# Optimization experiments

Hardware: AMD Instinct MI355X
Metric: run time of the kernel (lower is better)

## Reference

```python
import jax, jax.numpy as jnp
import numpy as np

B, N, F_IN, H, MH, STEPS = 8192, 9, 15, 128, 256, 4
E_PER = 16
MASK_IDX = jnp.arange(8)  # mask = [True]*8 + [False]


def setup_inputs() -> dict:
    key = jax.random.key(0)
    ks = jax.random.split(key, 24)
    s = 0.05
    inp = {
        "obs": jax.random.normal(ks[0], (B, 135), jnp.float32),
        "edges": jax.random.randint(ks[1], (B, 2, E_PER), 0, N, jnp.int32),
        "enc_W": jax.random.normal(ks[2], (F_IN, H), jnp.float32) * s,
        "enc_b": jax.random.normal(ks[3], (H,), jnp.float32) * s,
        "msg_W1": jax.random.normal(ks[4], (STEPS, 2 * H, MH), jnp.float32) * s,
        "msg_b1": jax.random.normal(ks[5], (STEPS, MH), jnp.float32) * s,
        "msg_W2": jax.random.normal(ks[6], (STEPS, MH, MH), jnp.float32) * s,
        "msg_b2": jax.random.normal(ks[7], (STEPS, MH), jnp.float32) * s,
        "msg_W3": jax.random.normal(ks[8], (STEPS, MH, H), jnp.float32) * s,
        "msg_b3": jax.random.normal(ks[9], (STEPS, H), jnp.float32) * s,
        "gru_Wi": jax.random.normal(ks[10], (STEPS, H, 3 * H), jnp.float32) * s,
        "gru_Wh": jax.random.normal(ks[11], (STEPS, H, 3 * H), jnp.float32) * s,
        "gru_bi": jax.random.normal(ks[12], (STEPS, 3 * H), jnp.float32) * s,
        "gru_bh": jax.random.normal(ks[13], (STEPS, 3 * H), jnp.float32) * s,
        "dec_W1": jax.random.normal(ks[14], (H, MH), jnp.float32) * s,
        "dec_b1": jax.random.normal(ks[15], (MH,), jnp.float32) * s,
        "dec_W2": jax.random.normal(ks[16], (MH, MH), jnp.float32) * s,
        "dec_b2": jax.random.normal(ks[17], (MH,), jnp.float32) * s,
        "dec_W3": jax.random.normal(ks[18], (MH, 1), jnp.float32) * s,
        "dec_b3": jax.random.normal(ks[19], (1,), jnp.float32) * s,
    }
    return inp


def reference(obs, edges, enc_W, enc_b, msg_W1, msg_b1, msg_W2, msg_b2,
              msg_W3, msg_b3, gru_Wi, gru_Wh, gru_bi, gru_bh,
              dec_W1, dec_b1, dec_W2, dec_b2, dec_W3, dec_b3):
    BN = B * N
    x = obs.reshape(BN, F_IN)                       # [B*N, 15]
    x = jnp.tanh(x @ enc_W + enc_b)                 # encoder -> [B*N, H]

    # flatten per-graph edges into a global edge list, then add self-loops
    offsets = (jnp.arange(B, dtype=jnp.int32) * N)[:, None, None]
    eg = edges + offsets                            # [B, 2, 16]
    loops = jnp.arange(BN, dtype=jnp.int32)
    src = jnp.concatenate([eg[:, 0, :].reshape(-1), loops])  # x_j (source)
    dst = jnp.concatenate([eg[:, 1, :].reshape(-1), loops])  # x_i (target)
    deg = jax.ops.segment_sum(jnp.ones_like(dst, dtype=x.dtype), dst,
                              num_segments=BN)      # >=1 due to self-loops

    for s in range(STEPS):
        m = jnp.concatenate([x[dst], x[src]], axis=-1)       # [E, 2H]
        m = jnp.tanh(m @ msg_W1[s] + msg_b1[s])
        m = jnp.tanh(m @ msg_W2[s] + msg_b2[s])
        m = m @ msg_W3[s] + msg_b3[s]                        # [E, H]
        aggr = jax.ops.segment_sum(m, dst, num_segments=BN) / deg[:, None]
        # GRUCell(input=aggr, hidden=x), PyTorch gate order (r, z, n)
        gi = aggr @ gru_Wi[s] + gru_bi[s]
        gh = x @ gru_Wh[s] + gru_bh[s]
        ir, iz, inn = jnp.split(gi, 3, axis=-1)
        hr, hz, hn = jnp.split(gh, 3, axis=-1)
        r = jax.nn.sigmoid(ir + hr)
        z = jax.nn.sigmoid(iz + hz)
        n = jnp.tanh(inn + r * hn)
        x = (1.0 - z) * n + z * x

    d = jnp.tanh(x @ dec_W1 + dec_b1)
    d = jnp.tanh(d @ dec_W2 + dec_b2)
    d = d @ dec_W3 + dec_b3                                  # [B*N, 1]
    out = d.reshape(B, N)
    return out[:, MASK_IDX]                                  # [B, 8]
```

## Files before the change

kernel.cpp:

```cpp
#include <hip/hip_runtime.h>
#include <hip/hip_bf16.h>
#include <math.h>

#define BGR   8192
#define NND   9
#define BN    73728
#define NE    131072
#define ETOT  204800
#define H     128
#define MH    256
#define FIN   15

typedef __bf16 bf16_t;
typedef bf16_t bf16x8 __attribute__((ext_vector_type(8)));
typedef float  f32x4  __attribute__((ext_vector_type(4)));
typedef float  f32x16 __attribute__((ext_vector_type(16)));

__device__ __forceinline__ unsigned short f2bf(float f) {
    unsigned int u = __float_as_uint(f);
    u += 0x7fff + ((u >> 16) & 1);
    return (unsigned short)(u >> 16);
}
__device__ __forceinline__ unsigned int pkbf(float a, float b) {
    union { __hip_bfloat162 h; unsigned int u; } un;
    un.h = __float22bfloat162_rn(make_float2(a, b));
    return un.u;
}
__device__ __forceinline__ bf16x8 as_frag(int4 v) {
    union { int4 i; bf16x8 f; } u; u.i = v; return u.f;
}
__device__ __forceinline__ float fast_tanh(float v) {
    float e = __expf(2.0f * v);
    return 1.0f - __fdividef(2.0f, e + 1.0f);
}
__device__ __forceinline__ int sw16(int m, int k) {
    return m * 256 + ((((k >> 3) ^ (m & 15)) << 3) | (k & 7));
}
__device__ __forceinline__ int swp(int m, int k) {
    return m * 128 + ((((k >> 3) ^ (m & 15)) << 3) | (k & 7));
}
__device__ __forceinline__ int sw_off(int m, int k) {
    return m * 256 + ((((k >> 3) ^ (m & 7)) << 3) | (k & 7));
}

__global__ void deg_kernel(const int* __restrict__ edges, float* __restrict__ inv_deg) {
    int g = blockIdx.x * 256 + threadIdx.x;
    if (g >= BGR) return;
    int cnt[NND];
#pragma unroll
    for (int n = 0; n < NND; ++n) cnt[n] = 1;
    for (int j = 0; j < 16; ++j) {
        int d = edges[g * 32 + 16 + j];
#pragma unroll
        for (int n = 0; n < NND; ++n) cnt[n] += (d == n) ? 1 : 0;
    }
#pragma unroll
    for (int n = 0; n < NND; ++n) inv_deg[g * NND + n] = 1.0f / (float)cnt[n];
}

__global__ void enc_kernel(const float* __restrict__ obs, const float* __restrict__ W,
                           const float* __restrict__ b, float* __restrict__ x) {
    int tid = blockIdx.x * 256 + threadIdx.x;
    int i = tid >> 7, h = tid & 127;
    float acc = b[h];
#pragma unroll
    for (int k = 0; k < FIN; ++k) acc += obs[i * FIN + k] * W[k * H + h];
    x[i * H + h] = tanhf(acc);
}

__global__ void wt_kernel(const float* __restrict__ W1, const float* __restrict__ W2,
                          const float* __restrict__ W3, const float* __restrict__ Wi,
                          const float* __restrict__ Wh, const float* __restrict__ dW1,
                          const float* __restrict__ dW2, unsigned short* __restrict__ out) {
    int idx = blockIdx.x * 256 + threadIdx.x;
    float v;
    if (idx < 262144) {
        int s = idx >> 16, r = idx & 65535, n = r >> 8, k = r & 255;
        v = W1[(s << 16) + (k << 8) + n];
    } else if (idx < 524288) {
        int i2 = idx - 262144;
        int s = i2 >> 16, r = i2 & 65535, n = r >> 8, k = r & 255;
        v = W2[(s << 16) + (k << 8) + n];
    } else if (idx < 655360) {
        int i3 = idx - 524288;
        int s = i3 >> 15, r = i3 & 32767, n = r >> 8, k = r & 255;
        v = W3[(s << 15) + (k << 7) + n];
    } else if (idx < 1179648) {
        int i4 = idx - 655360;
        int s = i4 >> 17, rr = i4 & 131071;
        int p = rr >> 8, k = rr & 255;
        int w = p >> 6, rem = p & 63;
        int gate = rem >> 4, c = rem & 15;
        int h = w * 16 + c;
        const int sb = s * 49152;
        if (gate == 0)      v = (k < 128) ? Wi[sb + k * 384 + h]       : Wh[sb + (k - 128) * 384 + h];
        else if (gate == 1) v = (k < 128) ? Wi[sb + k * 384 + 128 + h] : Wh[sb + (k - 128) * 384 + 128 + h];
        else if (gate == 2) v = (k < 128) ? Wi[sb + k * 384 + 256 + h] : 0.f;
        else                v = (k < 128) ? 0.f                        : Wh[sb + (k - 128) * 384 + 256 + h];
    } else if (idx < 1212416) {
        int i5 = idx - 1179648;
        int n = i5 >> 7, k = i5 & 127;
        v = dW1[k * 256 + n];
    } else if (idx < 1277952) {
        int i6 = idx - 1212416;
        int n = i6 >> 8, k = i6 & 255;
        v = dW2[k * 256 + n];
    } else {
        int i7 = idx - 1277952;
        int s = i7 >> 16, rr = i7 & 65535;
        int n = rr >> 7, k = rr & 127;
        v = (n < 256) ? W1[(s << 16) + (k << 8) + n]
                      : W1[(s << 16) + ((k + 128) << 8) + (n - 256)];
    }
    out[idx] = f2bf(v);
}

__global__ __launch_bounds__(512, 4) void proj_mfma(
        const float* __restrict__ x, const unsigned short* __restrict__ W1P,
        unsigned short* __restrict__ P) {
    __shared__ unsigned short lbuf[64 * 128];
    const int t = threadIdx.x;
    const int n0 = blockIdx.x * 64;
    const int wv = t >> 6, ln = t & 63, l31 = ln & 31, lh = ln >> 5;

    {
        const int m = t >> 3, q = t & 7;
        const float* xs = x + (size_t)(n0 + m) * H + q * 16;
#pragma unroll
        for (int i = 0; i < 4; ++i) {
            float4 v = *(const float4*)(xs + i * 4);
            uint2 o; o.x = pkbf(v.x, v.y); o.y = pkbf(v.z, v.w);
            *(uint2*)(lbuf + swp(m, q * 16 + i * 4)) = o;
        }
    }
    __syncthreads();

    f32x16 acc[2][2];
#pragma unroll
    for (int a = 0; a < 2; ++a)
#pragma unroll
        for (int b = 0; b < 2; ++b)
#pragma unroll
            for (int i = 0; i < 16; ++i) acc[a][b][i] = 0.f;

    const int nb = wv * 64;
    const unsigned short* wp0 = W1P + (size_t)(nb + l31) * 128 + lh * 8;
    const unsigned short* wp1 = W1P + (size_t)(nb + 32 + l31) * 128 + lh * 8;
#pragma unroll
    for (int ks = 0; ks < 8; ++ks) {
        const int kk = ks * 16 + lh * 8;
        bf16x8 a0 = as_frag(*(const int4*)(lbuf + swp(l31, kk)));
        bf16x8 a1 = as_frag(*(const int4*)(lbuf + swp(32 + l31, kk)));
        bf16x8 w0 = as_frag(*(const int4*)(wp0 + ks * 16));
        bf16x8 w1 = as_frag(*(const int4*)(wp1 + ks * 16));
        acc[0][0] = __builtin_amdgcn_mfma_f32_32x32x16_bf16(a0, w0, acc[0][0], 0, 0, 0);
        acc[0][1] = __builtin_amdgcn_mfma_f32_32x32x16_bf16(a0, w1, acc[0][1], 0, 0, 0);
        acc[1][0] = __builtin_amdgcn_mfma_f32_32x32x16_bf16(a1, w0, acc[1][0], 0, 0, 0);
        acc[1][1] = __builtin_amdgcn_mfma_f32_32x32x16_bf16(a1, w1, acc[1][1], 0, 0, 0);
    }

#pragma unroll
    for (int mt = 0; mt < 2; ++mt)
#pragma unroll
        for (int nt = 0; nt < 2; ++nt) {
            const int col = nb + nt * 32 + l31;
#pragma unroll
            for (int reg = 0; reg < 16; ++reg) {
                const int mrow = mt * 32 + (reg & 3) + ((reg >> 2) << 3) + (lh << 2);
                P[(size_t)(n0 + mrow) * 512 + col] = f2bf(acc[mt][nt][reg]);
            }
        }
}

__global__ __launch_bounds__(512, 4) void msg_mfma(
        const unsigned short* __restrict__ P, const int* __restrict__ edges,
        const float* __restrict__ b1,
        const unsigned short* __restrict__ W2T, const float* __restrict__ b2,
        const unsigned short* __restrict__ W3T,
        float* __restrict__ aggr) {
    __shared__ unsigned short bufA[64 * 256];
    __shared__ unsigned short bufB[64 * 256];
    __shared__ int sdst[64];
    const int t  = threadIdx.x;
    const int e0 = blockIdx.x * 64;
    const int wv = t >> 6;
    const int ln = t & 63;
    const int l31 = ln & 31;
    const int lh  = ln >> 5;

    if (t < 64) {
        const int eg = e0 + t;
        sdst[t] = (eg < NE) ? ((eg >> 4) * NND + edges[(eg >> 4) * 32 + 16 + (eg & 15)])
                            : (eg - NE);
    }
    {
        const int row = t >> 3;
        const int c0  = (t & 7) * 32;
        const int eg  = e0 + row;
        int dn, sn;
        if (eg < NE) {
            int g = eg >> 4, j = eg & 15;
            sn = g * NND + edges[g * 32 + j];
            dn = g * NND + edges[g * 32 + 16 + j];
        } else {
            dn = sn = eg - NE;
        }
        const unsigned short* up = P + (size_t)dn * 512 + c0;
        const unsigned short* vp = P + (size_t)sn * 512 + 256 + c0;
#pragma unroll
        for (int i = 0; i < 4; ++i) {
            const uint4 uu = *(const uint4*)(up + i * 8);
            const uint4 vv = *(const uint4*)(vp + i * 8);
            const unsigned int ua[4] = {uu.x, uu.y, uu.z, uu.w};
            const unsigned int va[4] = {vv.x, vv.y, vv.z, vv.w};
            unsigned int op[4];
#pragma unroll
            for (int j = 0; j < 4; ++j) {
                const float2 bb = *(const float2*)(b1 + c0 + i * 8 + j * 2);
                const float s0 = fast_tanh(__uint_as_float(ua[j] << 16) +
                                           __uint_as_float(va[j] << 16) + bb.x);
                const float s1 = fast_tanh(__uint_as_float(ua[j] & 0xffff0000u) +
                                           __uint_as_float(va[j] & 0xffff0000u) + bb.y);
                op[j] = pkbf(s0, s1);
            }
            *(uint4*)(bufA + sw16(row, c0 + i * 8)) = make_uint4(op[0], op[1], op[2], op[3]);
        }
    }
    __syncthreads();

    {
        f32x16 acc0, acc1;
#pragma unroll
        for (int i = 0; i < 16; ++i) { acc0[i] = 0.f; acc1[i] = 0.f; }
        const unsigned short* wp = W2T + (size_t)(wv * 32 + l31) * 256 + lh * 8;
#pragma unroll
        for (int ks = 0; ks < 16; ++ks) {
            const int kk = ks * 16 + lh * 8;
            bf16x8 a0 = as_frag(*(const int4*)(bufA + sw16(l31, kk)));
            bf16x8 a1 = as_frag(*(const int4*)(bufA + sw16(32 + l31, kk)));
            bf16x8 bw = as_frag(*(const int4*)(wp + ks * 16));
            acc0 = __builtin_amdgcn_mfma_f32_32x32x16_bf16(a0, bw, acc0, 0, 0, 0);
            acc1 = __builtin_amdgcn_mfma_f32_32x32x16_bf16(a1, bw, acc1, 0, 0, 0);
        }
        const int n = wv * 32 + l31;
        const float bias = b2[n];
#pragma unroll
        for (int reg = 0; reg < 16; ++reg) {
            const int mrow = (reg & 3) + ((reg >> 2) << 3) + (lh << 2);
            bufB[sw16(mrow, n)]      = f2bf(fast_tanh(acc0[reg] + bias));
            bufB[sw16(32 + mrow, n)] = f2bf(fast_tanh(acc1[reg] + bias));
        }
    }
    __syncthreads();

    {
        const int mt = wv & 1, nq = wv >> 1;
        const int n = nq * 32 + l31;
        f32x16 acc;
#pragma unroll
        for (int i = 0; i < 16; ++i) acc[i] = 0.f;
        const unsigned short* wp = W3T + (size_t)n * 256 + lh * 8;
#pragma unroll
        for (int ks = 0; ks < 16; ++ks) {
            const int kk = ks * 16 + lh * 8;
            bf16x8 a = as_frag(*(const int4*)(bufB + sw16(mt * 32 + l31, kk)));
            bf16x8 bw = as_frag(*(const int4*)(wp + ks * 16));
            acc = __builtin_amdgcn_mfma_f32_32x32x16_bf16(a, bw, acc, 0, 0, 0);
        }
#pragma unroll
        for (int reg = 0; reg < 16; ++reg) {
            const int m = mt * 32 + (reg & 3) + ((reg >> 2) << 3) + (lh << 2);
            atomicAdd(aggr + (size_t)sdst[m] * H + n, acc[reg]);
        }
    }
}

__global__ __launch_bounds__(512, 4) void gru_mfma(
        float* __restrict__ x, float* __restrict__ aggr, const float* __restrict__ inv_deg,
        const unsigned short* __restrict__ WG, const float* __restrict__ b3m,
        const float* __restrict__ bi, const float* __restrict__ bh) {
    __shared__ unsigned short bufA[64 * 256];
    const int t = threadIdx.x;
    const int n0 = blockIdx.x * 64;
    const int wv = t >> 6, ln = t & 63, lrow = ln & 15, lq = ln >> 4;

    {
        const int m = t >> 3;
        const int q = t & 7;
        const int k0 = q * 32;
        const int node = n0 + m;
        if (q < 4) {
            const float scale = inv_deg[node];
            const float* src = aggr + (size_t)node * H + k0;
#pragma unroll
            for (int i = 0; i < 8; ++i) {
                float4 v = *(const float4*)(src + i * 4);
                const float4 bb = *(const float4*)(b3m + k0 + i * 4);
                v.x = v.x * scale + bb.x; v.y = v.y * scale + bb.y;
                v.z = v.z * scale + bb.z; v.w = v.w * scale + bb.w;
                uint2 o; o.x = pkbf(v.x, v.y); o.y = pkbf(v.z, v.w);
                *(uint2*)(bufA + sw_off(m, k0 + i * 4)) = o;
            }
        } else {
            const float* src = x + (size_t)node * H + (k0 - 128);
#pragma unroll
            for (int i = 0; i < 8; ++i) {
                float4 v = *(const float4*)(src + i * 4);
                uint2 o; o.x = pkbf(v.x, v.y); o.y = pkbf(v.z, v.w);
                *(uint2*)(bufA + sw_off(m, k0 + i * 4)) = o;
            }
        }
    }
    __syncthreads();

    const f32x4 zero = {0.f, 0.f, 0.f, 0.f};
    f32x4 acc[4][4];
#pragma unroll
    for (int i = 0; i < 4; ++i)
#pragma unroll
        for (int j = 0; j < 4; ++j) acc[i][j] = zero;

    const unsigned short* wgp = WG + (size_t)(wv * 64 + lrow) * 256;
#pragma unroll
    for (int kq = 0; kq < 8; ++kq) {
        const int ko = kq * 32 + lq * 8;
        bf16x8 af[4], bfr[4];
#pragma unroll
        for (int tm = 0; tm < 4; ++tm)
            af[tm] = as_frag(*(const int4*)(bufA + sw_off(tm * 16 + lrow, ko)));
#pragma unroll
        for (int g = 0; g < 4; ++g)
            bfr[g] = as_frag(*(const int4*)(wgp + (size_t)g * 16 * 256 + ko));
#pragma unroll
        for (int tm = 0; tm < 4; ++tm)
#pragma unroll
            for (int g = 0; g < 4; ++g)
                acc[tm][g] = __builtin_amdgcn_mfma_f32_16x16x32_bf16(af[tm], bfr[g], acc[tm][g], 0, 0, 0);
    }

    {
        const int h = wv * 16 + lrow;
        const float b_r = bi[h] + bh[h];
        const float b_z = bi[128 + h] + bh[128 + h];
        const float b_n = bi[256 + h];
        const float b_h = bh[256 + h];
#pragma unroll
        for (int tm = 0; tm < 4; ++tm) {
#pragma unroll
            for (int r = 0; r < 4; ++r) {
                const int node = n0 + tm * 16 + lq * 4 + r;
                const float irhr = acc[tm][0][r] + b_r;
                const float izhz = acc[tm][1][r] + b_z;
                const float inn  = acc[tm][2][r] + b_n;
                const float hn   = acc[tm][3][r] + b_h;
                const float rg = 1.f / (1.f + expf(-irhr));
                const float zg = 1.f / (1.f + expf(-izhz));
                const float ng = tanhf(inn + rg * hn);
                const float xo = x[(size_t)node * H + h];
                x[(size_t)node * H + h] = (1.f - zg) * ng + zg * xo;
                aggr[(size_t)node * H + h] = 0.f;
            }
        }
    }
}

__global__ __launch_bounds__(256, 4) void dec_mfma(
        const float* __restrict__ x,
        const unsigned short* __restrict__ W1T, const float* __restrict__ b1,
        const unsigned short* __restrict__ W2T, const float* __restrict__ b2,
        const float* __restrict__ W3, const float* __restrict__ b3,
        float* __restrict__ out) {
    __shared__ unsigned short buf[64 * 256];
    const int t = threadIdx.x;
    const int id0 = blockIdx.x * 64;
    const int wv = t >> 6, ln = t & 63, lrow = ln & 15, lq = ln >> 4;
    const int nbase = wv * 64;

    {
        const int m = t >> 2, q = t & 3;
        const int id = id0 + m;
        const int node = (id >> 3) * NND + (id & 7);
        const float* src = x + (size_t)node * H + q * 32;
#pragma unroll
        for (int i = 0; i < 8; ++i) {
            float4 v = *(const float4*)(src + i * 4);
            uint2 o; o.x = pkbf(v.x, v.y); o.y = pkbf(v.z, v.w);
            *(uint2*)(buf + sw_off(m, q * 32 + i * 4)) = o;
        }
    }
    __syncthreads();

    const f32x4 zero = {0.f, 0.f, 0.f, 0.f};

    {
        f32x4 acc[4][4];
#pragma unroll
        for (int i = 0; i < 4; ++i)
#pragma unroll
            for (int j = 0; j < 4; ++j) acc[i][j] = zero;
#pragma unroll
        for (int kq = 0; kq < 4; ++kq) {
            const int ko = kq * 32 + lq * 8;
            bf16x8 af[4], bfr[4];
#pragma unroll
            for (int tm = 0; tm < 4; ++tm)
                af[tm] = as_frag(*(const int4*)(buf + sw_off(tm * 16 + lrow, ko)));
#pragma unroll
            for (int tn = 0; tn < 4; ++tn)
                bfr[tn] = as_frag(*(const int4*)(W1T + (size_t)(nbase + tn * 16 + lrow) * 128 + ko));
#pragma unroll
            for (int tm = 0; tm < 4; ++tm)
#pragma unroll
                for (int tn = 0; tn < 4; ++tn)
                    acc[tm][tn] = __builtin_amdgcn_mfma_f32_16x16x32_bf16(af[tm], bfr[tn], acc[tm][tn], 0, 0, 0);
        }
        __syncthreads();
#pragma unroll
        for (int tn = 0; tn < 4; ++tn) {
            const int n = nbase + tn * 16 + lrow;
            const float bias = b1[n];
#pragma unroll
            for (int tm = 0; tm < 4; ++tm)
#pragma unroll
                for (int r = 0; r < 4; ++r) {
                    const int m = tm * 16 + lq * 4 + r;
                    buf[sw_off(m, n)] = f2bf(fast_tanh(acc[tm][tn][r] + bias));
                }
        }
    }
    __syncthreads();

    {
        f32x4 acc[4][4];
#pragma unroll
        for (int i = 0; i < 4; ++i)
#pragma unroll
            for (int j = 0; j < 4; ++j) acc[i][j] = zero;
#pragma unroll
        for (int kq = 0; kq < 8; ++kq) {
            const int ko = kq * 32 + lq * 8;
            bf16x8 af[4], bfr[4];
#pragma unroll
            for (int tm = 0; tm < 4; ++tm)
                af[tm] = as_frag(*(const int4*)(buf + sw_off(tm * 16 + lrow, ko)));
#pragma unroll
            for (int tn = 0; tn < 4; ++tn)
                bfr[tn] = as_frag(*(const int4*)(W2T + (size_t)(nbase + tn * 16 + lrow) * 256 + ko));
#pragma unroll
            for (int tm = 0; tm < 4; ++tm)
#pragma unroll
                for (int tn = 0; tn < 4; ++tn)
                    acc[tm][tn] = __builtin_amdgcn_mfma_f32_16x16x32_bf16(af[tm], bfr[tn], acc[tm][tn], 0, 0, 0);
        }
        __syncthreads();
#pragma unroll
        for (int tn = 0; tn < 4; ++tn) {
            const int n = nbase + tn * 16 + lrow;
            const float bias = b2[n];
#pragma unroll
            for (int tm = 0; tm < 4; ++tm)
#pragma unroll
                for (int r = 0; r < 4; ++r) {
                    const int m = tm * 16 + lq * 4 + r;
                    buf[sw_off(m, n)] = f2bf(fast_tanh(acc[tm][tn][r] + bias));
                }
        }
    }
    __syncthreads();

    {
        const int m = t >> 2, p = t & 3;
        float s = 0.f;
#pragma unroll
        for (int i = 0; i < 64; ++i) {
            const int k = p * 64 + i;
            const float a = __uint_as_float((unsigned int)buf[sw_off(m, k)] << 16);
            s += a * W3[k];
        }
        s += __shfl_xor(s, 1);
        s += __shfl_xor(s, 2);
        if (p == 0) out[id0 + m] = s + b3[0];
    }
}

extern "C" void kernel_launch(void* const* d_in, const int* in_sizes, int n_in,
                              void* d_out, int out_size, void* d_ws, size_t ws_size,
                              hipStream_t stream) {
    const float* obs    = (const float*)d_in[0];
    const int*   edges  = (const int*)  d_in[1];
    const float* enc_W  = (const float*)d_in[2];
    const float* enc_b  = (const float*)d_in[3];
    const float* msg_W1 = (const float*)d_in[4];
    const float* msg_b1 = (const float*)d_in[5];
    const float* msg_W2 = (const float*)d_in[6];
    const float* msg_b2 = (const float*)d_in[7];
    const float* msg_W3 = (const float*)d_in[8];
    const float* msg_b3 = (const float*)d_in[9];
    const float* gru_Wi = (const float*)d_in[10];
    const float* gru_Wh = (const float*)d_in[11];
    const float* gru_bi = (const float*)d_in[12];
    const float* gru_bh = (const float*)d_in[13];
    const float* dec_W1 = (const float*)d_in[14];
    const float* dec_b1 = (const float*)d_in[15];
    const float* dec_W2 = (const float*)d_in[16];
    const float* dec_b2 = (const float*)d_in[17];
    const float* dec_W3 = (const float*)d_in[18];
    const float* dec_b3 = (const float*)d_in[19];

    float* x       = (float*)d_ws;
    float* aggr    = x + (size_t)BN * H;
    float* inv_deg = aggr + (size_t)BN * H;
    unsigned short* wbf = (unsigned short*)(inv_deg + BN);
    unsigned short* P   = wbf + 1540096;

    hipMemsetAsync(aggr, 0, (size_t)BN * H * sizeof(float), stream);
    deg_kernel<<<(BGR + 255) / 256, 256, 0, stream>>>(edges, inv_deg);
    wt_kernel<<<1540096 / 256, 256, 0, stream>>>(msg_W1, msg_W2, msg_W3, gru_Wi, gru_Wh,
                                                 dec_W1, dec_W2, wbf);
    enc_kernel<<<BN * H / 256, 256, 0, stream>>>(obs, enc_W, enc_b, x);

    for (int s = 0; s < 4; ++s) {
        const unsigned short* W2T = wbf + 262144 + (size_t)s * 65536;
        const unsigned short* W3T = wbf + 524288 + (size_t)s * 32768;
        const unsigned short* WGs = wbf + 655360 + (size_t)s * 131072;
        const unsigned short* W1P = wbf + 1277952 + (size_t)s * 65536;
        proj_mfma<<<BN / 64, 512, 0, stream>>>(x, W1P, P);
        msg_mfma<<<ETOT / 64, 512, 0, stream>>>(
            P, edges,
            msg_b1 + (size_t)s * 256,
            W2T, msg_b2 + (size_t)s * 256,
            W3T,
            aggr);
        gru_mfma<<<BN / 64, 512, 0, stream>>>(
            x, aggr, inv_deg, WGs, msg_b3 + (size_t)s * 128,
            gru_bi + (size_t)s * 384, gru_bh + (size_t)s * 384);
    }

    dec_mfma<<<BGR * 8 / 64, 256, 0, stream>>>(
        x, wbf + 1179648, dec_b1, wbf + 1212416, dec_b2, dec_W3, dec_b3, (float*)d_out);
}
```

Baseline: 1.351 ms.

## Fuse self-loop messages into projection kernel and aggregate edges in shared memory

The self-loop edges, one per node, are now computed inside the projection kernel. It runs the full 3-layer message MLP on each node's own projections and writes the result straight into aggr, so the memset and the per-step zeroing in the GRU kernel are no longer needed. The edge kernel then handles only the real edges. Each 64-edge block covers exactly 4 graphs (36 nodes), so it scatter-adds into a shared-memory tile and does one non-atomic read-modify-write to global memory, replacing global atomics. This depends on the projection kernel having initialised aggr first and on each block owning a disjoint set of graph nodes.

```diff
diff --git a/kernel.cpp b/kernel.cpp
--- a/kernel.cpp
+++ b/kernel.cpp
@@ -6,7 +6,6 @@
 #define NND   9
 #define BN    73728
 #define NE    131072
-#define ETOT  204800
 #define H     128
 #define MH    256
 #define FIN   15
@@ -108,17 +107,23 @@
     } else {
         int i7 = idx - 1277952;
         int s = i7 >> 16, rr = i7 & 65535;
-        int n = rr >> 7, k = rr & 127;
-        v = (n < 256) ? W1[(s << 16) + (k << 8) + n]
-                      : W1[(s << 16) + ((k + 128) << 8) + (n - 256)];
+        int p = rr >> 7, k = rr & 127;
+        int w = p >> 6, rem = p & 63;
+        int side = rem >> 5, c = rem & 31;
+        int n = w * 32 + c;
+        v = W1[(s << 16) + ((k + side * 128) << 8) + n];
     }
     out[idx] = f2bf(v);
 }
 
 __global__ __launch_bounds__(512, 4) void proj_mfma(
         const float* __restrict__ x, const unsigned short* __restrict__ W1P,
-        unsigned short* __restrict__ P) {
+        const float* __restrict__ b1,
+        const unsigned short* __restrict__ W2T, const float* __restrict__ b2,
+        const unsigned short* __restrict__ W3T,
+        unsigned short* __restrict__ P, float* __restrict__ aggr) {
     __shared__ unsigned short lbuf[64 * 128];
+    __shared__ unsigned short abuf[64 * 256];
     const int t = threadIdx.x;
     const int n0 = blockIdx.x * 64;
     const int wv = t >> 6, ln = t & 63, l31 = ln & 31, lh = ln >> 5;
@@ -135,41 +140,87 @@
     }
     __syncthreads();
 
-    f32x16 acc[2][2];
-#pragma unroll
-    for (int a = 0; a < 2; ++a)
-#pragma unroll
-        for (int b = 0; b < 2; ++b)
-#pragma unroll
-            for (int i = 0; i < 16; ++i) acc[a][b][i] = 0.f;
-
-    const int nb = wv * 64;
-    const unsigned short* wp0 = W1P + (size_t)(nb + l31) * 128 + lh * 8;
-    const unsigned short* wp1 = W1P + (size_t)(nb + 32 + l31) * 128 + lh * 8;
-#pragma unroll
-    for (int ks = 0; ks < 8; ++ks) {
-        const int kk = ks * 16 + lh * 8;
-        bf16x8 a0 = as_frag(*(const int4*)(lbuf + swp(l31, kk)));
-        bf16x8 a1 = as_frag(*(const int4*)(lbuf + swp(32 + l31, kk)));
-        bf16x8 w0 = as_frag(*(const int4*)(wp0 + ks * 16));
-        bf16x8 w1 = as_frag(*(const int4*)(wp1 + ks * 16));
-        acc[0][0] = __builtin_amdgcn_mfma_f32_32x32x16_bf16(a0, w0, acc[0][0], 0, 0, 0);
-        acc[0][1] = __builtin_amdgcn_mfma_f32_32x32x16_bf16(a0, w1, acc[0][1], 0, 0, 0);
-        acc[1][0] = __builtin_amdgcn_mfma_f32_32x32x16_bf16(a1, w0, acc[1][0], 0, 0, 0);
-        acc[1][1] = __builtin_amdgcn_mfma_f32_32x32x16_bf16(a1, w1, acc[1][1], 0, 0, 0);
-    }
-
-#pragma unroll
-    for (int mt = 0; mt < 2; ++mt)
-#pragma unroll
-        for (int nt = 0; nt < 2; ++nt) {
-            const int col = nb + nt * 32 + l31;
+    {
+        f32x16 au[2], av[2];
+#pragma unroll
+        for (int a = 0; a < 2; ++a)
+#pragma unroll
+            for (int i = 0; i < 16; ++i) { au[a][i] = 0.f; av[a][i] = 0.f; }
+        const unsigned short* wpu = W1P + (size_t)(wv * 64 + l31) * 128 + lh * 8;
+        const unsigned short* wpv = W1P + (size_t)(wv * 64 + 32 + l31) * 128 + lh * 8;
+#pragma unroll
+        for (int ks = 0; ks < 8; ++ks) {
+            const int kk = ks * 16 + lh * 8;
+            bf16x8 a0 = as_frag(*(const int4*)(lbuf + swp(l31, kk)));
+            bf16x8 a1 = as_frag(*(const int4*)(lbuf + swp(32 + l31, kk)));
+            bf16x8 wu = as_frag(*(const int4*)(wpu + ks * 16));
+            bf16x8 wvv = as_frag(*(const int4*)(wpv + ks * 16));
+            au[0] = __builtin_amdgcn_mfma_f32_32x32x16_bf16(a0, wu, au[0], 0, 0, 0);
+            au[1] = __builtin_amdgcn_mfma_f32_32x32x16_bf16(a1, wu, au[1], 0, 0, 0);
+            av[0] = __builtin_amdgcn_mfma_f32_32x32x16_bf16(a0, wvv, av[0], 0, 0, 0);
+            av[1] = __builtin_amdgcn_mfma_f32_32x32x16_bf16(a1, wvv, av[1], 0, 0, 0);
+        }
+        const int n = wv * 32 + l31;
+        const float bias = b1[n];
+#pragma unroll
+        for (int mt = 0; mt < 2; ++mt)
 #pragma unroll
             for (int reg = 0; reg < 16; ++reg) {
                 const int mrow = mt * 32 + (reg & 3) + ((reg >> 2) << 3) + (lh << 2);
-                P[(size_t)(n0 + mrow) * 512 + col] = f2bf(acc[mt][nt][reg]);
+                const size_t node = n0 + mrow;
+                P[node * 512 + n]       = f2bf(au[mt][reg]);
+                P[node * 512 + 256 + n] = f2bf(av[mt][reg]);
+                abuf[sw16(mrow, n)] = f2bf(fast_tanh(au[mt][reg] + av[mt][reg] + bias));
             }
-        }
+    }
+    __syncthreads();
+
+    {
+        f32x16 acc0, acc1;
+#pragma unroll
+        for (int i = 0; i < 16; ++i) { acc0[i] = 0.f; acc1[i] = 0.f; }
+        const unsigned short* wp = W2T + (size_t)(wv * 32 + l31) * 256 + lh * 8;
+#pragma unroll
+        for (int ks = 0; ks < 16; ++ks) {
+            const int kk = ks * 16 + lh * 8;
+            bf16x8 a0 = as_frag(*(const int4*)(abuf + sw16(l31, kk)));
+            bf16x8 a1 = as_frag(*(const int4*)(abuf + sw16(32 + l31, kk)));
+            bf16x8 bw = as_frag(*(const int4*)(wp + ks * 16));
+            acc0 = __builtin_amdgcn_mfma_f32_32x32x16_bf16(a0, bw, acc0, 0, 0, 0);
+            acc1 = __builtin_amdgcn_mfma_f32_32x32x16_bf16(a1, bw, acc1, 0, 0, 0);
+        }
+        __syncthreads();
+        const int n = wv * 32 + l31;
+        const float bias = b2[n];
+#pragma unroll
+        for (int reg = 0; reg < 16; ++reg) {
+            const int mrow = (reg & 3) + ((reg >> 2) << 3) + (lh << 2);
+            abuf[sw16(mrow, n)]      = f2bf(fast_tanh(acc0[reg] + bias));
+            abuf[sw16(32 + mrow, n)] = f2bf(fast_tanh(acc1[reg] + bias));
+        }
+    }
+    __syncthreads();
+
+    {
+        const int mt = wv & 1, nq = wv >> 1;
+        const int n = nq * 32 + l31;
+        f32x16 acc;
+#pragma unroll
+        for (int i = 0; i < 16; ++i) acc[i] = 0.f;
+        const unsigned short* wp = W3T + (size_t)n * 256 + lh * 8;
+#pragma unroll
+        for (int ks = 0; ks < 16; ++ks) {
+            const int kk = ks * 16 + lh * 8;
+            bf16x8 a = as_frag(*(const int4*)(abuf + sw16(mt * 32 + l31, kk)));
+            bf16x8 bw = as_frag(*(const int4*)(wp + ks * 16));
+            acc = __builtin_amdgcn_mfma_f32_32x32x16_bf16(a, bw, acc, 0, 0, 0);
+        }
+#pragma unroll
+        for (int reg = 0; reg < 16; ++reg) {
+            const int m = mt * 32 + (reg & 3) + ((reg >> 2) << 3) + (lh << 2);
+            aggr[(size_t)(n0 + m) * H + n] = acc[reg];
+        }
+    }
 }
 
 __global__ __launch_bounds__(512, 4) void msg_mfma(
@@ -180,7 +231,7 @@
         float* __restrict__ aggr) {
     __shared__ unsigned short bufA[64 * 256];
     __shared__ unsigned short bufB[64 * 256];
-    __shared__ int sdst[64];
+    __shared__ unsigned char sdstL[64];
     const int t  = threadIdx.x;
     const int e0 = blockIdx.x * 64;
     const int wv = t >> 6;
@@ -190,21 +241,15 @@
 
     if (t < 64) {
         const int eg = e0 + t;
-        sdst[t] = (eg < NE) ? ((eg >> 4) * NND + edges[(eg >> 4) * 32 + 16 + (eg & 15)])
-                            : (eg - NE);
+        sdstL[t] = (unsigned char)(((eg >> 4) & 3) * NND + edges[(eg >> 4) * 32 + 16 + (eg & 15)]);
     }
     {
         const int row = t >> 3;
         const int c0  = (t & 7) * 32;
         const int eg  = e0 + row;
-        int dn, sn;
-        if (eg < NE) {
-            int g = eg >> 4, j = eg & 15;
-            sn = g * NND + edges[g * 32 + j];
-            dn = g * NND + edges[g * 32 + 16 + j];
-        } else {
-            dn = sn = eg - NE;
-        }
+        const int g = eg >> 4, j = eg & 15;
+        const int sn = g * NND + edges[g * 32 + j];
+        const int dn = g * NND + edges[g * 32 + 16 + j];
         const unsigned short* up = P + (size_t)dn * 512 + c0;
         const unsigned short* vp = P + (size_t)sn * 512 + 256 + c0;
 #pragma unroll
@@ -215,13 +260,13 @@
             const unsigned int va[4] = {vv.x, vv.y, vv.z, vv.w};
             unsigned int op[4];
 #pragma unroll
-            for (int j = 0; j < 4; ++j) {
-                const float2 bb = *(const float2*)(b1 + c0 + i * 8 + j * 2);
-                const float s0 = fast_tanh(__uint_as_float(ua[j] << 16) +
-                                           __uint_as_float(va[j] << 16) + bb.x);
-                const float s1 = fast_tanh(__uint_as_float(ua[j] & 0xffff0000u) +
-                                           __uint_as_float(va[j] & 0xffff0000u) + bb.y);
-                op[j] = pkbf(s0, s1);
+            for (int j2 = 0; j2 < 4; ++j2) {
+                const float2 bb = *(const float2*)(b1 + c0 + i * 8 + j2 * 2);
+                const float s0 = fast_tanh(__uint_as_float(ua[j2] << 16) +
+                                           __uint_as_float(va[j2] << 16) + bb.x);
+                const float s1 = fast_tanh(__uint_as_float(ua[j2] & 0xffff0000u) +
+                                           __uint_as_float(va[j2] & 0xffff0000u) + bb.y);
+                op[j2] = pkbf(s0, s1);
             }
             *(uint4*)(bufA + sw16(row, c0 + i * 8)) = make_uint4(op[0], op[1], op[2], op[3]);
         }
@@ -253,6 +298,11 @@
     }
     __syncthreads();
 
+    float* aL = (float*)bufA;
+#pragma unroll
+    for (int i = 0; i < 9; ++i) aL[i * 512 + t] = 0.f;
+    __syncthreads();
+
     {
         const int mt = wv & 1, nq = wv >> 1;
         const int n = nq * 32 + l31;
@@ -270,7 +320,17 @@
 #pragma unroll
         for (int reg = 0; reg < 16; ++reg) {
             const int m = mt * 32 + (reg & 3) + ((reg >> 2) << 3) + (lh << 2);
-            atomicAdd(aggr + (size_t)sdst[m] * H + n, acc[reg]);
+            atomicAdd(&aL[(int)sdstL[m] * 128 + n], acc[reg]);
+        }
+    }
+    __syncthreads();
+
+    {
+        float* gp = aggr + (size_t)blockIdx.x * 36 * 128;
+#pragma unroll
+        for (int i = 0; i < 9; ++i) {
+            const int idx = i * 512 + t;
+            gp[idx] += aL[idx];
         }
     }
 }
@@ -358,7 +418,6 @@
                 const float ng = tanhf(inn + rg * hn);
                 const float xo = x[(size_t)node * H + h];
                 x[(size_t)node * H + h] = (1.f - zg) * ng + zg * xo;
-                aggr[(size_t)node * H + h] = 0.f;
             }
         }
     }
@@ -513,7 +572,6 @@
     unsigned short* wbf = (unsigned short*)(inv_deg + BN);
     unsigned short* P   = wbf + 1540096;
 
-    hipMemsetAsync(aggr, 0, (size_t)BN * H * sizeof(float), stream);
     deg_kernel<<<(BGR + 255) / 256, 256, 0, stream>>>(edges, inv_deg);
     wt_kernel<<<1540096 / 256, 256, 0, stream>>>(msg_W1, msg_W2, msg_W3, gru_Wi, gru_Wh,
                                                  dec_W1, dec_W2, wbf);
@@ -524,8 +582,10 @@
         const unsigned short* W3T = wbf + 524288 + (size_t)s * 32768;
         const unsigned short* WGs = wbf + 655360 + (size_t)s * 131072;
         const unsigned short* W1P = wbf + 1277952 + (size_t)s * 65536;
-        proj_mfma<<<BN / 64, 512, 0, stream>>>(x, W1P, P);
-        msg_mfma<<<ETOT / 64, 512, 0, stream>>>(
+        proj_mfma<<<BN / 64, 512, 0, stream>>>(
+            x, W1P, msg_b1 + (size_t)s * 256,
+            W2T, msg_b2 + (size_t)s * 256, W3T, P, aggr);
+        msg_mfma<<<NE / 64, 512, 0, stream>>>(
             P, edges,
             msg_b1 + (size_t)s * 256,
             W2T, msg_b2 + (size_t)s * 256,
```

Measured after the change: 1.499 ms. 1.11x slower.
